# Performance work log

Measured on AMD Instinct MI355X. Metric: run time of the kernel, lower is better.

## Reference

```python
import jax, jax.numpy as jnp
import numpy as np

EPS = 1e-5

def rmsnorm(x, w, eps=EPS):
    v = jnp.mean(x * x, axis=-1, keepdims=True)
    return x * jax.lax.rsqrt(v + eps) * w

def setup_inputs() -> dict:
    key = jax.random.key(0)
    B, L, H, D, N, R, K = 4, 2048, 2048, 4096, 16, 128, 4
    ks = jax.random.split(key, 10)
    f = lambda k, shape, s=0.02: jax.random.normal(k, shape, jnp.float32) * s
    return dict(
        hidden_states=jax.random.normal(ks[0], (B, L, H), jnp.float32),
        residual=jax.random.normal(ks[1], (B, L, H), jnp.float32),
        norm_weight=jnp.ones((H,), jnp.float32),
        in_proj_w=f(ks[2], (2 * D, H)),
        conv_w=f(ks[3], (D, 1, K), 0.1),
        conv_b=jnp.zeros((D,), jnp.float32),
        x_proj_w=f(ks[4], (R + 2 * N, D)),
        dt_proj_w=f(ks[5], (D, R), 0.05),
        dt_proj_b=jnp.full((D,), -2.0, jnp.float32) + f(ks[6], (D,), 0.1),
        A_log=jnp.log(jnp.broadcast_to(jnp.arange(1, N + 1, dtype=jnp.float32), (D, N))),
        D_param=jnp.ones((D,), jnp.float32),
        out_proj_w=f(ks[7], (H, D)),
    )

def reference(hidden_states, residual, norm_weight, in_proj_w, conv_w, conv_b,
              x_proj_w, dt_proj_w, dt_proj_b, A_log, D_param, out_proj_w):
    # fused residual-add + RMSNorm (vLLM RMSNorm(x, residual) semantics)
    x = hidden_states + residual
    residual = x
    x = rmsnorm(x, norm_weight)

    D = in_proj_w.shape[0] // 2
    N = A_log.shape[1]
    R = dt_proj_w.shape[1]
    K = conv_w.shape[-1]

    # in_proj -> x, z gate
    xz = jnp.einsum('blh,dh->bld', x, in_proj_w)  # [B,L,2D]
    xs, z = xz[..., :D], xz[..., D:]

    # depthwise causal conv1d over time + SiLU
    xc = jnp.transpose(xs, (0, 2, 1))  # [B,D,L]
    xc = jax.lax.conv_general_dilated(
        xc, conv_w, (1,), [(K - 1, 0)],
        dimension_numbers=('NCH', 'OIH', 'NCH'), feature_group_count=D)
    xc = jax.nn.silu(xc + conv_b[None, :, None])
    xs = jnp.transpose(xc, (0, 2, 1))  # [B,L,D]

    # x_proj -> dt (low rank), B, C
    dbl = jnp.einsum('bld,ed->ble', xs, x_proj_w)
    dt_in, Bm, Cm = dbl[..., :R], dbl[..., R:R + N], dbl[..., R + N:]
    dt = jax.nn.softplus(jnp.einsum('blr,dr->bld', dt_in, dt_proj_w) + dt_proj_b)

    A = -jnp.exp(A_log)  # [D,N]

    # selective scan, time-major
    dt_t = jnp.transpose(dt, (1, 0, 2))   # [L,B,D]
    x_t = jnp.transpose(xs, (1, 0, 2))    # [L,B,D]
    B_t = jnp.transpose(Bm, (1, 0, 2))    # [L,B,N]
    C_t = jnp.transpose(Cm, (1, 0, 2))    # [L,B,N]
    Bsz = xs.shape[0]
    h0 = jnp.zeros((Bsz, D, N), jnp.float32)

    def step(h, inp):
        dti, xi, Bi, Ci = inp
        dA = jnp.exp(dti[:, :, None] * A)                       # [B,D,N]
        h = dA * h + (dti * xi)[:, :, None] * Bi[:, None, :]
        y = jnp.einsum('bdn,bn->bd', h, Ci)
        return h, y

    _, ys = jax.lax.scan(step, h0, (dt_t, x_t, B_t, C_t))  # ys: [L,B,D]
    y = jnp.transpose(ys, (1, 0, 2)) + xs * D_param
    y = y * jax.nn.silu(z)
    out = jnp.einsum('bld,hd->blh', y, out_proj_w)
    return out, residual
```

## Files before the change

### kernel.cpp

```cpp
#include <hip/hip_runtime.h>

typedef __bf16 bf16;
typedef __bf16 bf16x8 __attribute__((ext_vector_type(8)));
typedef float  f32x4  __attribute__((ext_vector_type(4)));

#define B_  4
#define L_  2048
#define H_  2048
#define D_  4096
#define N_  16
#define R_  128
#define M_  (B_ * L_)

typedef __attribute__((address_space(1))) const void GV;
typedef __attribute__((address_space(3))) void SV;
__device__ __forceinline__ void async_cp16(const void* g, void* s) {
    __builtin_amdgcn_global_load_lds((GV*)g, (SV*)s, 16, 0, 0);
}

__global__ __launch_bounds__(256) void cast_kernel(
    const float* __restrict__ src, bf16* __restrict__ dst)
{
    const size_t i = ((size_t)blockIdx.x * 256 + threadIdx.x) * 8;
    float4 a = *(const float4*)(src + i);
    float4 b = *(const float4*)(src + i + 4);
    bf16x8 o;
    o[0] = (bf16)a.x; o[1] = (bf16)a.y; o[2] = (bf16)a.z; o[3] = (bf16)a.w;
    o[4] = (bf16)b.x; o[5] = (bf16)b.y; o[6] = (bf16)b.z; o[7] = (bf16)b.w;
    *(bf16x8*)(dst + i) = o;
}

__global__ __launch_bounds__(256) void add_rmsnorm_kernel(
    const float* __restrict__ hs, const float* __restrict__ res,
    const float* __restrict__ w, float* __restrict__ resid_out,
    bf16* __restrict__ xnorm)
{
    const int m = blockIdx.x;
    const int t = threadIdx.x;
    const size_t base = (size_t)m * H_ + t * 8;
    float4 h0 = *(const float4*)(hs + base);
    float4 h1 = *(const float4*)(hs + base + 4);
    float4 r0 = *(const float4*)(res + base);
    float4 r1 = *(const float4*)(res + base + 4);
    float x[8];
    x[0] = h0.x + r0.x; x[1] = h0.y + r0.y; x[2] = h0.z + r0.z; x[3] = h0.w + r0.w;
    x[4] = h1.x + r1.x; x[5] = h1.y + r1.y; x[6] = h1.z + r1.z; x[7] = h1.w + r1.w;
    float ss = 0.f;
#pragma unroll
    for (int i = 0; i < 8; ++i) ss += x[i] * x[i];
#pragma unroll
    for (int off = 32; off > 0; off >>= 1) ss += __shfl_down(ss, off, 64);
    __shared__ float red[4];
    if ((t & 63) == 0) red[t >> 6] = ss;
    __syncthreads();
    float tot = red[0] + red[1] + red[2] + red[3];
    float rs = rsqrtf(tot * (1.0f / H_) + 1e-5f);
    float4 w0 = *(const float4*)(w + t * 8);
    float4 w1 = *(const float4*)(w + t * 8 + 4);
    float wv[8] = {w0.x, w0.y, w0.z, w0.w, w1.x, w1.y, w1.z, w1.w};
    *(float4*)(resid_out + base)     = make_float4(x[0], x[1], x[2], x[3]);
    *(float4*)(resid_out + base + 4) = make_float4(x[4], x[5], x[6], x[7]);
    bf16x8 xo;
#pragma unroll
    for (int i = 0; i < 8; ++i) xo[i] = (bf16)(x[i] * rs * wv[i]);
    *(bf16x8*)(xnorm + base) = xo;
}

template <int EPI>
__global__ __launch_bounds__(256) void gemm_bt(
    const bf16* __restrict__ A, const bf16* __restrict__ Bm,
    int N, int K,
    bf16* __restrict__ Cb, bf16* __restrict__ aux_b, float* __restrict__ aux_f,
    const float* __restrict__ bias)
{
    __shared__ __align__(16) bf16 As[128 * 32];
    __shared__ __align__(16) bf16 Bs[128 * 32];

    const int t  = threadIdx.x;
    const int m0 = blockIdx.y * 128;
    const int n0 = blockIdx.x * 128;

    const int fa = t * 8;
    const int ra = fa >> 5;
    const int ca = fa & 31;

    const int wave = t >> 6, lane = t & 63;
    const int wm = (wave >> 1) * 64, wn = (wave & 1) * 64;
    const int lr = lane & 15, quad = lane >> 4;

    int rb0 = n0 + ra;      if (rb0 > N - 1) rb0 = N - 1;
    int rb1 = n0 + 64 + ra; if (rb1 > N - 1) rb1 = N - 1;

    f32x4 acc[4][4] = {};

    for (int k0 = 0; k0 < K; k0 += 32) {
        __syncthreads();
        async_cp16(A  + (size_t)(m0 + ra) * K + k0 + ca,      As + fa);
        async_cp16(A  + (size_t)(m0 + 64 + ra) * K + k0 + ca, As + 2048 + fa);
        async_cp16(Bm + (size_t)rb0 * K + k0 + ca,            Bs + fa);
        async_cp16(Bm + (size_t)rb1 * K + k0 + ca,            Bs + 2048 + fa);
        __syncthreads();

        bf16x8 af[4], bf[4];
#pragma unroll
        for (int i = 0; i < 4; ++i)
            af[i] = *(const bf16x8*)&As[(wm + i * 16 + lr) * 32 + quad * 8];
#pragma unroll
        for (int i = 0; i < 4; ++i)
            bf[i] = *(const bf16x8*)&Bs[(wn + i * 16 + lr) * 32 + quad * 8];
#pragma unroll
        for (int mi = 0; mi < 4; ++mi)
#pragma unroll
            for (int ni = 0; ni < 4; ++ni)
                acc[mi][ni] = __builtin_amdgcn_mfma_f32_16x16x32_bf16(
                    af[mi], bf[ni], acc[mi][ni], 0, 0, 0);
    }

#pragma unroll
    for (int mi = 0; mi < 4; ++mi) {
#pragma unroll
        for (int ni = 0; ni < 4; ++ni) {
            const int row = m0 + wm + mi * 16 + quad * 4;
            const int col = n0 + wn + ni * 16 + lr;
            if (EPI == 0) {
#pragma unroll
                for (int r = 0; r < 4; ++r)
                    Cb[(size_t)(row + r) * N + col] = (bf16)acc[mi][ni][r];
            } else if (EPI == 1) {
                if (col < 128) {
#pragma unroll
                    for (int r = 0; r < 4; ++r)
                        aux_b[(size_t)(row + r) * 128 + col] = (bf16)acc[mi][ni][r];
                } else if (col < 160) {
#pragma unroll
                    for (int r = 0; r < 4; ++r)
                        aux_f[(size_t)(row + r) * 32 + (col - 128)] = acc[mi][ni][r];
                }
            } else if (EPI == 2) {
                float bv = bias[col];
#pragma unroll
                for (int r = 0; r < 4; ++r) {
                    float v = acc[mi][ni][r] + bv;
                    v = fmaxf(v, 0.f) + log1pf(expf(-fabsf(v)));
                    Cb[(size_t)(row + r) * N + col] = (bf16)v;
                }
            } else {
#pragma unroll
                for (int r = 0; r < 4; ++r)
                    aux_f[(size_t)(row + r) * N + col] = acc[mi][ni][r];
            }
        }
    }
}

__global__ __launch_bounds__(256) void conv_silu_kernel(
    const bf16* __restrict__ xs, const float* __restrict__ cw,
    const float* __restrict__ cb, bf16* __restrict__ xc)
{
    const size_t idx = (size_t)blockIdx.x * 256 + threadIdx.x;
    const int d = (int)(idx & (D_ - 1));
    const int m = (int)(idx >> 12);
    const int l = m & (L_ - 1);
    float acc = cb[d];
    const float* wp = cw + (size_t)d * 4;
#pragma unroll
    for (int k = 0; k < 4; ++k) {
        int j = l + k - 3;
        if (j >= 0)
            acc += wp[k] * (float)xs[(size_t)(m + k - 3) * D_ + d];
    }
    acc = acc * __builtin_amdgcn_rcpf(1.f + __expf(-acc));
    xc[idx] = (bf16)acc;
}

__global__ __launch_bounds__(256) void scan_kernel(
    const bf16* dt, const bf16* __restrict__ xc,
    const float* __restrict__ bc, const bf16* __restrict__ zb,
    const float* __restrict__ A_log, const float* __restrict__ Dp,
    bf16* y)
{
    const int t   = threadIdx.x;
    const int grp = blockIdx.x * 32 + (t >> 3);
    const int n2  = (t & 7) * 2;
    const int b   = grp >> 12;
    const int d   = grp & (D_ - 1);
    const bool w0 = (t & 7) == 0;

    float2 Al = *(const float2*)(A_log + (size_t)d * 16 + n2);
    const float A0 = -__expf(Al.x);
    const float A1 = -__expf(Al.y);
    const float Dpar = Dp[d];

    float h0 = 0.f, h1 = 0.f;

    const size_t eb = (size_t)b * L_ * D_ + d;
    const bf16*  dtp = dt + eb;
    const bf16*  xcp = xc + eb;
    const bf16*  zbp = zb + eb;
    bf16*        yp  = y  + eb;
    const float* bcp = bc + (size_t)b * L_ * 32 + n2;

    float  dta = (float)dtp[0],   dtb = (float)dtp[D_];
    float  xca = (float)xcp[0],   xcb = (float)xcp[D_];
    float  zba = (float)zbp[0],   zbb = (float)zbp[D_];
    float2 Ba  = *(const float2*)(bcp),       Bb = *(const float2*)(bcp + 32);
    float2 Ca  = *(const float2*)(bcp + 16),  Cb = *(const float2*)(bcp + 48);

    const bf16*  pfd = dtp + 2 * (size_t)D_;
    const bf16*  pfx = xcp + 2 * (size_t)D_;
    const bf16*  pfz = zbp + 2 * (size_t)D_;
    const float* pfb = bcp + 64;

#define SCAN_STEP()                                                          \
    {                                                                        \
        const float dtx = dta * xca;                                         \
        const float a0 = __expf(dta * A0);                                   \
        const float a1 = __expf(dta * A1);                                   \
        h0 = fmaf(a0, h0, dtx * Ba.x);                                       \
        h1 = fmaf(a1, h1, dtx * Ba.y);                                       \
        float pv = fmaf(h1, Ca.y, h0 * Ca.x);                                \
        pv += __shfl_xor(pv, 1, 64);                                         \
        pv += __shfl_xor(pv, 2, 64);                                         \
        pv += __shfl_xor(pv, 4, 64);                                         \
        const float sz = zba * __builtin_amdgcn_rcpf(1.f + __expf(-zba));    \
        const float yv = (pv + xca * Dpar) * sz;                             \
        if (w0) *yp = (bf16)yv;                                              \
        yp += D_;                                                            \
    }

    for (int l = 0; l < L_ - 2; ++l) {
        float  dtn = (float)*pfd;  pfd += D_;
        float  xcn = (float)*pfx;  pfx += D_;
        float  zbn = (float)*pfz;  pfz += D_;
        float2 Bn  = *(const float2*)(pfb);
        float2 Cn  = *(const float2*)(pfb + 16);
        pfb += 32;
        SCAN_STEP();
        dta = dtb; dtb = dtn;
        xca = xcb; xcb = xcn;
        zba = zbb; zbb = zbn;
        Ba = Bb; Bb = Bn;
        Ca = Cb; Cb = Cn;
    }
    SCAN_STEP();
    dta = dtb; xca = xcb; zba = zbb; Ba = Bb; Ca = Cb;
    SCAN_STEP();
#undef SCAN_STEP
}

extern "C" void kernel_launch(void* const* d_in, const int* in_sizes, int n_in,
                              void* d_out, int out_size, void* d_ws, size_t ws_size,
                              hipStream_t stream)
{
    const float* hs    = (const float*)d_in[0];
    const float* res   = (const float*)d_in[1];
    const float* nw    = (const float*)d_in[2];
    const float* w_in  = (const float*)d_in[3];
    const float* cw    = (const float*)d_in[4];
    const float* cb    = (const float*)d_in[5];
    const float* w_xp  = (const float*)d_in[6];
    const float* w_dt  = (const float*)d_in[7];
    const float* b_dt  = (const float*)d_in[8];
    const float* Alog  = (const float*)d_in[9];
    const float* Dpar  = (const float*)d_in[10];
    const float* w_out = (const float*)d_in[11];

    float* out       = (float*)d_out;
    float* resid_out = out + (size_t)M_ * H_;

    char* ws = (char*)d_ws;
    bf16*  xsbuf   = (bf16*)(ws);
    bf16*  dtbuf   = (bf16*)(ws);
    bf16*  ybuf    = dtbuf;
    bf16*  zbuf    = (bf16*)(ws + 67108864ull);
    bf16*  w_out_b = (bf16*)(ws + 67108864ull);
    bf16*  xnorm   = (bf16*)(ws + 134217728ull);
    bf16*  w_in_b  = (bf16*)(ws + 167772160ull);
    bf16*  xconv   = (bf16*)(ws + 134217728ull);
    bf16*  dtin    = (bf16*)(ws + 201326592ull);
    float* bcbuf   = (float*)(ws + 203423744ull);
    bf16*  w_xp_b  = (bf16*)(ws + 204472320ull);
    bf16*  w_dt_b  = (bf16*)(ws + 205783040ull);

    cast_kernel<<<16777216 / 2048, 256, 0, stream>>>(w_in, w_in_b);
    cast_kernel<<<655360   / 2048, 256, 0, stream>>>(w_xp, w_xp_b);
    cast_kernel<<<524288   / 2048, 256, 0, stream>>>(w_dt, w_dt_b);

    add_rmsnorm_kernel<<<M_, 256, 0, stream>>>(hs, res, nw, resid_out, xnorm);

    gemm_bt<0><<<dim3(32, 64), 256, 0, stream>>>(xnorm, w_in_b, 4096, 2048,
                                                 xsbuf, nullptr, nullptr, nullptr);
    gemm_bt<0><<<dim3(32, 64), 256, 0, stream>>>(xnorm, w_in_b + (size_t)4096 * 2048, 4096, 2048,
                                                 zbuf, nullptr, nullptr, nullptr);

    conv_silu_kernel<<<(M_ * D_) / 256, 256, 0, stream>>>(xsbuf, cw, cb, xconv);

    gemm_bt<1><<<dim3(2, 64), 256, 0, stream>>>(xconv, w_xp_b, 160, 4096,
                                                nullptr, dtin, bcbuf, nullptr);

    gemm_bt<2><<<dim3(32, 64), 256, 0, stream>>>(dtin, w_dt_b, 4096, 128,
                                                 dtbuf, nullptr, nullptr, b_dt);

    scan_kernel<<<512, 256, 0, stream>>>(dtbuf, xconv, bcbuf, zbuf, Alog, Dpar, ybuf);

    cast_kernel<<<8388608 / 2048, 256, 0, stream>>>(w_out, w_out_b);

    gemm_bt<3><<<dim3(16, 64), 256, 0, stream>>>(ybuf, w_out_b, 2048, 4096,
                                                 nullptr, nullptr, out, nullptr);
}
```

Measured before the change: 1.905 ms.

## Fuse SiLU(z) into in_proj GEMM epilogue and unroll scan by four

Adds a GEMM epilogue that applies SiLU to the z half of in_proj, so the scan kernel reads the precomputed gate instead of evaluating sigmoid on every step. The scan loop is restructured to process four timesteps per iteration, with a four-deep register prefetch, batched shuffle reductions, and 32-bit offsets. This is meant to cut transcendental work on the serial scan path and give more memory-level parallelism for its strided loads, at the cost of more registers per thread.

```diff
diff --git a/kernel.cpp b/kernel.cpp
--- a/kernel.cpp
+++ b/kernel.cpp
@@ -144,10 +144,17 @@
                     v = fmaxf(v, 0.f) + log1pf(expf(-fabsf(v)));
                     Cb[(size_t)(row + r) * N + col] = (bf16)v;
                 }
-            } else {
+            } else if (EPI == 3) {
 #pragma unroll
                 for (int r = 0; r < 4; ++r)
                     aux_f[(size_t)(row + r) * N + col] = acc[mi][ni][r];
+            } else {
+#pragma unroll
+                for (int r = 0; r < 4; ++r) {
+                    float v = acc[mi][ni][r];
+                    v = v * __builtin_amdgcn_rcpf(1.f + __expf(-v));
+                    Cb[(size_t)(row + r) * N + col] = (bf16)v;
+                }
             }
         }
     }
@@ -175,7 +182,7 @@
 
 __global__ __launch_bounds__(256) void scan_kernel(
     const bf16* dt, const bf16* __restrict__ xc,
-    const float* __restrict__ bc, const bf16* __restrict__ zb,
+    const float* __restrict__ bc, const bf16* __restrict__ sz,
     const float* __restrict__ A_log, const float* __restrict__ Dp,
     bf16* y)
 {
@@ -193,59 +200,68 @@
 
     float h0 = 0.f, h1 = 0.f;
 
-    const size_t eb = (size_t)b * L_ * D_ + d;
-    const bf16*  dtp = dt + eb;
-    const bf16*  xcp = xc + eb;
-    const bf16*  zbp = zb + eb;
-    bf16*        yp  = y  + eb;
-    const float* bcp = bc + (size_t)b * L_ * 32 + n2;
-
-    float  dta = (float)dtp[0],   dtb = (float)dtp[D_];
-    float  xca = (float)xcp[0],   xcb = (float)xcp[D_];
-    float  zba = (float)zbp[0],   zbb = (float)zbp[D_];
-    float2 Ba  = *(const float2*)(bcp),       Bb = *(const float2*)(bcp + 32);
-    float2 Ca  = *(const float2*)(bcp + 16),  Cb = *(const float2*)(bcp + 48);
-
-    const bf16*  pfd = dtp + 2 * (size_t)D_;
-    const bf16*  pfx = xcp + 2 * (size_t)D_;
-    const bf16*  pfz = zbp + 2 * (size_t)D_;
-    const float* pfb = bcp + 64;
-
-#define SCAN_STEP()                                                          \
-    {                                                                        \
-        const float dtx = dta * xca;                                         \
-        const float a0 = __expf(dta * A0);                                   \
-        const float a1 = __expf(dta * A1);                                   \
-        h0 = fmaf(a0, h0, dtx * Ba.x);                                       \
-        h1 = fmaf(a1, h1, dtx * Ba.y);                                       \
-        float pv = fmaf(h1, Ca.y, h0 * Ca.x);                                \
-        pv += __shfl_xor(pv, 1, 64);                                         \
-        pv += __shfl_xor(pv, 2, 64);                                         \
-        pv += __shfl_xor(pv, 4, 64);                                         \
-        const float sz = zba * __builtin_amdgcn_rcpf(1.f + __expf(-zba));    \
-        const float yv = (pv + xca * Dpar) * sz;                             \
-        if (w0) *yp = (bf16)yv;                                              \
-        yp += D_;                                                            \
-    }
-
-    for (int l = 0; l < L_ - 2; ++l) {
-        float  dtn = (float)*pfd;  pfd += D_;
-        float  xcn = (float)*pfx;  pfx += D_;
-        float  zbn = (float)*pfz;  pfz += D_;
-        float2 Bn  = *(const float2*)(pfb);
-        float2 Cn  = *(const float2*)(pfb + 16);
-        pfb += 32;
-        SCAN_STEP();
-        dta = dtb; dtb = dtn;
-        xca = xcb; xcb = xcn;
-        zba = zbb; zbb = zbn;
-        Ba = Bb; Bb = Bn;
-        Ca = Cb; Cb = Cn;
-    }
-    SCAN_STEP();
-    dta = dtb; xca = xcb; zba = zbb; Ba = Bb; Ca = Cb;
-    SCAN_STEP();
-#undef SCAN_STEP
+    const size_t bL = (size_t)b * L_ * D_;
+    const bf16*  dtb_ = dt + bL;
+    const bf16*  xcb_ = xc + bL;
+    const bf16*  szb_ = sz + bL;
+    bf16*        yb_  = y  + bL;
+    const float* bcb_ = bc + (size_t)b * L_ * 32 + n2;
+
+    unsigned off  = (unsigned)d;
+    unsigned boff = 0;
+
+    float  pdt[4], pxc[4], psz[4];
+    float2 pB[4], pC[4];
+#pragma unroll
+    for (int j = 0; j < 4; ++j) {
+        pdt[j] = (float)dtb_[off + j * D_];
+        pxc[j] = (float)xcb_[off + j * D_];
+        psz[j] = (float)szb_[off + j * D_];
+        pB[j]  = *(const float2*)(bcb_ + j * 32);
+        pC[j]  = *(const float2*)(bcb_ + 16 + j * 32);
+    }
+
+    for (int l4 = 0; l4 < L_; l4 += 4) {
+        const unsigned offn  = off  + 4u * D_;
+        const unsigned boffn = boff + 128u;
+        const bool pf = (l4 + 4 < L_);
+
+        float pv[4], xv[4], sv[4];
+#pragma unroll
+        for (int j = 0; j < 4; ++j) {
+            const float  dta = pdt[j];
+            const float  xca = pxc[j];
+            const float2 Ba  = pB[j];
+            const float2 Ca  = pC[j];
+            sv[j] = psz[j];
+            xv[j] = xca;
+            if (pf) {
+                pdt[j] = (float)dtb_[offn + j * D_];
+                pxc[j] = (float)xcb_[offn + j * D_];
+                psz[j] = (float)szb_[offn + j * D_];
+                pB[j]  = *(const float2*)(bcb_ + boffn + j * 32);
+                pC[j]  = *(const float2*)(bcb_ + boffn + 16 + j * 32);
+            }
+            const float dtx = dta * xca;
+            const float a0  = __expf(dta * A0);
+            const float a1  = __expf(dta * A1);
+            h0 = fmaf(a0, h0, dtx * Ba.x);
+            h1 = fmaf(a1, h1, dtx * Ba.y);
+            pv[j] = fmaf(h1, Ca.y, h0 * Ca.x);
+        }
+#pragma unroll
+        for (int j = 0; j < 4; ++j) pv[j] += __shfl_xor(pv[j], 1, 64);
+#pragma unroll
+        for (int j = 0; j < 4; ++j) pv[j] += __shfl_xor(pv[j], 2, 64);
+#pragma unroll
+        for (int j = 0; j < 4; ++j) pv[j] += __shfl_xor(pv[j], 4, 64);
+        if (w0) {
+#pragma unroll
+            for (int j = 0; j < 4; ++j)
+                yb_[off + j * D_] = (bf16)((pv[j] + xv[j] * Dpar) * sv[j]);
+        }
+        off = offn; boff = boffn;
+    }
 }
 
 extern "C" void kernel_launch(void* const* d_in, const int* in_sizes, int n_in,
@@ -290,7 +306,7 @@
 
     gemm_bt<0><<<dim3(32, 64), 256, 0, stream>>>(xnorm, w_in_b, 4096, 2048,
                                                  xsbuf, nullptr, nullptr, nullptr);
-    gemm_bt<0><<<dim3(32, 64), 256, 0, stream>>>(xnorm, w_in_b + (size_t)4096 * 2048, 4096, 2048,
+    gemm_bt<4><<<dim3(32, 64), 256, 0, stream>>>(xnorm, w_in_b + (size_t)4096 * 2048, 4096, 2048,
                                                  zbuf, nullptr, nullptr, nullptr);
 
     conv_silu_kernel<<<(M_ * D_) / 256, 256, 0, stream>>>(xsbuf, cw, cb, xconv);
```

Measured after the change: 2.195 ms. 1.15x slower.
